# Kernel optimization log

Hardware: AMD Instinct MI355X
Metric: run time of the kernel (lower is better)

Reference implementation:

```python
import jax, jax.numpy as jnp
import numpy as np

N_NODES = 100000
N_EDGES = 1600000
D_IN = 128
D_OUT = 128


def setup_inputs() -> dict:
    key = jax.random.key(0)
    k1, k2, k3, k4, k5 = jax.random.split(key, 5)
    h = jax.random.normal(k1, (N_NODES, D_IN), dtype=jnp.float32)
    src = jax.random.randint(k2, (N_EDGES,), 0, N_NODES, dtype=jnp.int64)
    dst = jax.random.randint(k3, (N_EDGES,), 0, N_NODES, dtype=jnp.int64)
    # Glorot-ish init for linear weights (PyTorch nn.Linear style: [out, in])
    scale = 1.0 / np.sqrt(D_IN)
    W_self = jax.random.uniform(k4, (D_OUT, D_IN), jnp.float32, -scale, scale)
    W_neigh = jax.random.uniform(k5, (D_OUT, D_IN), jnp.float32, -scale, scale)
    b = jnp.zeros((D_OUT,), dtype=jnp.float32)
    return {"h": h, "src": src, "dst": dst, "W_self": W_self,
            "W_neigh": W_neigh, "b": b}


def reference(h, src, dst, W_self, W_neigh, b):
    n_nodes = h.shape[0]
    # neighbor gather + segment-mean over in-neighbors (DGL fn.copy_u + fn.mean)
    msg = h[src]                                            # [E, D_in]
    neigh_sum = jax.ops.segment_sum(msg, dst, num_segments=n_nodes)
    deg = jax.ops.segment_sum(jnp.ones_like(dst, dtype=h.dtype), dst,
                              num_segments=n_nodes)         # [N]
    h_neigh = neigh_sum / jnp.maximum(deg, 1.0)[:, None]    # mean; 0 for isolated
    # SAGEConv mean: fc_self(h) + fc_neigh(h_neigh) + bias
    out = h @ W_self.T + h_neigh @ W_neigh.T + b
    return out
```

## Files before the change

### kernel.cpp

```cpp
#include <hip/hip_runtime.h>
#include <stdint.h>

#define NN 100000
#define NE 1600000
#define DD 128
#define NTILES ((NN + 127) / 128)
#define NB 256
#define CHUNK (NE / NB)
#define NBUCK ((NN + 255) / 256)
#define GH_N (NBUCK * NB)
#define GH_BLK (GH_N / 256)

typedef __bf16 bf16x8 __attribute__((ext_vector_type(8)));
typedef float f32x4 __attribute__((ext_vector_type(4)));
typedef float f32x2 __attribute__((ext_vector_type(2)));

__device__ __forceinline__ unsigned int f2bf2(float a, float b) {
  union { float f; unsigned u; } x, y;
  x.f = a; y.f = b;
  unsigned ua = x.u + (0x7FFFu + ((x.u >> 16) & 1u));
  unsigned ub = y.u + (0x7FFFu + ((y.u >> 16) & 1u));
  return (ua >> 16) | (ub & 0xFFFF0000u);
}

__global__ __launch_bounds__(256) void convert_h8_kernel(const float4* __restrict__ hp,
                                                         uint2* __restrict__ h8) {
  int gid = blockIdx.x * 256 + threadIdx.x;
  float4 a = hp[2 * gid], b = hp[2 * gid + 1];
  int lo = __builtin_amdgcn_cvt_pk_fp8_f32(a.x, a.y, 0, false);
  lo = __builtin_amdgcn_cvt_pk_fp8_f32(a.z, a.w, lo, true);
  int hi = __builtin_amdgcn_cvt_pk_fp8_f32(b.x, b.y, 0, false);
  hi = __builtin_amdgcn_cvt_pk_fp8_f32(b.z, b.w, hi, true);
  h8[gid] = make_uint2((unsigned)lo, (unsigned)hi);
}

__global__ __launch_bounds__(256) void coarse_hist_kernel(const int* __restrict__ dst,
                                                          int* __restrict__ gh) {
  __shared__ int lh[NBUCK];
  int t = threadIdx.x, b = blockIdx.x;
  for (int i = t; i < NBUCK; i += 256) lh[i] = 0;
  __syncthreads();
  int e0 = b * CHUNK;
  for (int e = e0 + t; e < e0 + CHUNK; e += 256)
    atomicAdd(&lh[dst[e] >> 8], 1);
  __syncthreads();
  for (int i = t; i < NBUCK; i += 256) gh[i * NB + b] = lh[i];
}

__global__ __launch_bounds__(256) void blocksum_kernel(const int* __restrict__ gh,
                                                       int* __restrict__ bsum) {
  __shared__ int s[256];
  int t = threadIdx.x;
  s[t] = gh[blockIdx.x * 256 + t];
  __syncthreads();
  for (int d = 128; d > 0; d >>= 1) {
    if (t < d) s[t] += s[t + d];
    __syncthreads();
  }
  if (t == 0) bsum[blockIdx.x] = s[0];
}

__global__ __launch_bounds__(512) void scanbsum_kernel(const int* __restrict__ bsum,
                                                       int* __restrict__ bsum_ex) {
  __shared__ int s[512];
  int t = threadIdx.x;
  int v = (t < GH_BLK) ? bsum[t] : 0;
  s[t] = v;
  __syncthreads();
  for (int d = 1; d < 512; d <<= 1) {
    int x = (t >= d) ? s[t - d] : 0;
    __syncthreads();
    s[t] += x;
    __syncthreads();
  }
  if (t < GH_BLK) bsum_ex[t] = s[t] - v;
}

__global__ __launch_bounds__(256) void scanfull_kernel(const int* __restrict__ gh,
                                                       const int* __restrict__ bsum_ex,
                                                       int* __restrict__ gsc) {
  __shared__ int s[256];
  int t = threadIdx.x;
  int idx = blockIdx.x * 256 + t;
  int v = gh[idx];
  s[t] = v;
  __syncthreads();
  for (int d = 1; d < 256; d <<= 1) {
    int x = (t >= d) ? s[t - d] : 0;
    __syncthreads();
    s[t] += x;
    __syncthreads();
  }
  gsc[idx] = bsum_ex[blockIdx.x] + s[t] - v;
}

__global__ __launch_bounds__(256) void coarse_scatter_kernel(
    const int* __restrict__ src, const int* __restrict__ dst,
    const int* __restrict__ gsc, unsigned* __restrict__ ebuf) {
  __shared__ int lhpad[512];
  __shared__ int lbase[NBUCK];
  __shared__ int lcur[NBUCK];
  __shared__ int gstart[NBUCK];
  __shared__ unsigned sdata[CHUNK];
  __shared__ int sgpos[CHUNK];
  int t = threadIdx.x, b = blockIdx.x;
  lhpad[t] = 0;
  lhpad[t + 256] = 0;
  __syncthreads();
  int e0 = b * CHUNK;
  for (int e = e0 + t; e < e0 + CHUNK; e += 256)
    atomicAdd(&lhpad[dst[e] >> 8], 1);
  __syncthreads();
  int cnt0 = lhpad[t], cnt1 = lhpad[t + 256];
  for (int d = 1; d < 512; d <<= 1) {
    int x0 = (t >= d) ? lhpad[t - d] : 0;
    int x1 = ((t + 256) >= d) ? lhpad[t + 256 - d] : 0;
    __syncthreads();
    lhpad[t] += x0;
    lhpad[t + 256] += x1;
    __syncthreads();
  }
  if (t < NBUCK) { lbase[t] = lhpad[t] - cnt0; lcur[t] = 0; gstart[t] = gsc[t * NB + b]; }
  int i2 = t + 256;
  if (i2 < NBUCK) { lbase[i2] = lhpad[i2] - cnt1; lcur[i2] = 0; gstart[i2] = gsc[i2 * NB + b]; }
  __syncthreads();
  for (int e = e0 + t; e < e0 + CHUNK; e += 256) {
    int d = dst[e], s = src[e];
    int bk = d >> 8;
    int slot = atomicAdd(&lcur[bk], 1);
    int lp = lbase[bk] + slot;
    sdata[lp] = ((unsigned)(d & 255) << 24) | (unsigned)s;
    sgpos[lp] = gstart[bk] + slot;
  }
  __syncthreads();
  for (int j = t; j < CHUNK; j += 256) ebuf[sgpos[j]] = sdata[j];
}

__global__ __launch_bounds__(256) void fine_sort_kernel(const unsigned* __restrict__ ebuf,
                                                        const int* __restrict__ gsc,
                                                        int* __restrict__ csr,
                                                        int* __restrict__ offs) {
  __shared__ int hist[256], scn[256], cur[256];
  int t = threadIdx.x, g = blockIdx.x;
  int base = gsc[g * NB];
  int end = (g == NBUCK - 1) ? NE : gsc[(g + 1) * NB];
  hist[t] = 0;
  __syncthreads();
  for (int j = base + t; j < end; j += 256)
    atomicAdd(&hist[ebuf[j] >> 24], 1);
  __syncthreads();
  int v = hist[t];
  scn[t] = v;
  __syncthreads();
  for (int d = 1; d < 256; d <<= 1) {
    int x = (t >= d) ? scn[t - d] : 0;
    __syncthreads();
    scn[t] += x;
    __syncthreads();
  }
  int excl = scn[t] - v;
  int node = g * 256 + t;
  if (node < NN) offs[node] = base + excl;
  if (node == NN - 1) offs[NN] = NE;
  cur[t] = excl;
  __syncthreads();
  for (int j = base + t; j < end; j += 256) {
    unsigned p = ebuf[j];
    int pos = atomicAdd(&cur[p >> 24], 1);
    csr[base + pos] = (int)(p & 0x00FFFFFFu);
  }
}

__device__ __forceinline__ void acc16(float* a, uint4 u) {
  f32x2 p;
  p = __builtin_amdgcn_cvt_pk_f32_fp8(u.x, false); a[0] += p.x;  a[1] += p.y;
  p = __builtin_amdgcn_cvt_pk_f32_fp8(u.x, true);  a[2] += p.x;  a[3] += p.y;
  p = __builtin_amdgcn_cvt_pk_f32_fp8(u.y, false); a[4] += p.x;  a[5] += p.y;
  p = __builtin_amdgcn_cvt_pk_f32_fp8(u.y, true);  a[6] += p.x;  a[7] += p.y;
  p = __builtin_amdgcn_cvt_pk_f32_fp8(u.z, false); a[8] += p.x;  a[9] += p.y;
  p = __builtin_amdgcn_cvt_pk_f32_fp8(u.z, true);  a[10] += p.x; a[11] += p.y;
  p = __builtin_amdgcn_cvt_pk_f32_fp8(u.w, false); a[12] += p.x; a[13] += p.y;
  p = __builtin_amdgcn_cvt_pk_f32_fp8(u.w, true);  a[14] += p.x; a[15] += p.y;
}

__global__ __launch_bounds__(256) void gather_kernel(const uint4* __restrict__ h8,
                                                     const int* __restrict__ offs,
                                                     const int* __restrict__ csr,
                                                     uint4* __restrict__ hneighbf4) {
  int q = (blockIdx.x * 256 + threadIdx.x) >> 3;
  int l = threadIdx.x & 7;
  if (q >= NN) return;
  int off0 = offs[q], off1 = offs[q + 1];
  float a[16];
#pragma unroll
  for (int i = 0; i < 16; i++) a[i] = 0.f;
  int j = off0;
  for (; j + 4 <= off1; j += 4) {
    int s0 = csr[j], s1 = csr[j + 1], s2 = csr[j + 2], s3 = csr[j + 3];
    uint4 u0 = h8[(size_t)s0 * 8 + l];
    uint4 u1 = h8[(size_t)s1 * 8 + l];
    uint4 u2 = h8[(size_t)s2 * 8 + l];
    uint4 u3 = h8[(size_t)s3 * 8 + l];
    acc16(a, u0); acc16(a, u1); acc16(a, u2); acc16(a, u3);
  }
  for (; j < off1; j++) acc16(a, h8[(size_t)csr[j] * 8 + l]);
  int deg = off1 - off0;
  float sc = (deg > 0) ? (1.0f / (float)deg) : 0.0f;
  uint4 r0, r1;
  r0.x = f2bf2(a[0] * sc, a[1] * sc);   r0.y = f2bf2(a[2] * sc, a[3] * sc);
  r0.z = f2bf2(a[4] * sc, a[5] * sc);   r0.w = f2bf2(a[6] * sc, a[7] * sc);
  r1.x = f2bf2(a[8] * sc, a[9] * sc);   r1.y = f2bf2(a[10] * sc, a[11] * sc);
  r1.z = f2bf2(a[12] * sc, a[13] * sc); r1.w = f2bf2(a[14] * sc, a[15] * sc);
  hneighbf4[(size_t)q * 16 + 2 * l] = r0;
  hneighbf4[(size_t)q * 16 + 2 * l + 1] = r1;
}

__device__ __forceinline__ void stage_f32(const float* __restrict__ X,
                                          int row0, int nvalid,
                                          uint4* buf, int t) {
#pragma unroll
  for (int i = 0; i < 8; i++) {
    int id = t + (i << 8);
    int r = id >> 4;
    int c8 = id & 15;
    int row = row0 + r;
    float4 v0 = {0.f, 0.f, 0.f, 0.f}, v1 = {0.f, 0.f, 0.f, 0.f};
    if (row < nvalid) {
      const float4* p = (const float4*)(X + (size_t)row * DD + (c8 << 3));
      v0 = p[0];
      v1 = p[1];
    }
    uint4 q;
    q.x = f2bf2(v0.x, v0.y);
    q.y = f2bf2(v0.z, v0.w);
    q.z = f2bf2(v1.x, v1.y);
    q.w = f2bf2(v1.z, v1.w);
    int rt = r >> 4, m = r & 15, kc = c8 >> 2, quad = c8 & 3;
    buf[(((rt << 2) + kc) << 6) + (quad << 4) + m] = q;
  }
}

__device__ __forceinline__ void stage_bf(const uint4* __restrict__ X,
                                         int row0, int nvalid,
                                         uint4* buf, int t) {
#pragma unroll
  for (int i = 0; i < 8; i++) {
    int d = t + (i << 8);
    int rt = d >> 8, kc = (d >> 6) & 3, quad = (d >> 4) & 3, m = d & 15;
    int r = rt * 16 + m, c8 = kc * 4 + quad;
    int row = row0 + r;
    uint4 q = {0u, 0u, 0u, 0u};
    if (row < nvalid) q = X[(size_t)row * 16 + c8];
    buf[d] = q;
  }
}

__device__ __forceinline__ void compute_half(const uint4* sA, const uint4* sW,
                                             f32x4 acc[2][8], int wv, int lane) {
#pragma unroll
  for (int kc = 0; kc < 4; kc++) {
    bf16x8 b[8];
#pragma unroll
    for (int n = 0; n < 8; n++)
      b[n] = *(const bf16x8*)&sW[(((n << 2) + kc) << 6) + lane];
    bf16x8 a0 = *(const bf16x8*)&sA[((((wv * 2 + 0) << 2) + kc) << 6) + lane];
    bf16x8 a1 = *(const bf16x8*)&sA[((((wv * 2 + 1) << 2) + kc) << 6) + lane];
#pragma unroll
    for (int n = 0; n < 8; n++) {
      acc[0][n] = __builtin_amdgcn_mfma_f32_16x16x32_bf16(a0, b[n], acc[0][n], 0, 0, 0);
      acc[1][n] = __builtin_amdgcn_mfma_f32_16x16x32_bf16(a1, b[n], acc[1][n], 0, 0, 0);
    }
  }
}

__global__ __launch_bounds__(256) void gemm_kernel(
    const float* __restrict__ h, const uint4* __restrict__ hneighbf,
    const float* __restrict__ Wself, const float* __restrict__ Wneigh,
    const float* __restrict__ bias, float* __restrict__ out) {
  __shared__ uint4 sA[2048];
  __shared__ uint4 sW[2048];
  int t = threadIdx.x;
  int wv = t >> 6;
  int lane = t & 63;
  int row0 = blockIdx.x * 128;

  f32x4 acc[2][8];
#pragma unroll
  for (int i = 0; i < 2; i++)
#pragma unroll
    for (int n = 0; n < 8; n++) acc[i][n] = f32x4{0.f, 0.f, 0.f, 0.f};

  stage_f32(h, row0, NN, sA, t);
  stage_f32(Wself, 0, 128, sW, t);
  __syncthreads();
  compute_half(sA, sW, acc, wv, lane);
  __syncthreads();

  stage_bf(hneighbf, row0, NN, sA, t);
  stage_f32(Wneigh, 0, 128, sW, t);
  __syncthreads();
  compute_half(sA, sW, acc, wv, lane);

  int col = lane & 15, rq = lane >> 4;
  float bv[8];
#pragma unroll
  for (int n = 0; n < 8; n++) bv[n] = bias[n * 16 + col];
#pragma unroll
  for (int rt = 0; rt < 2; rt++) {
    int rb = row0 + (wv * 2 + rt) * 16 + rq * 4;
#pragma unroll
    for (int r = 0; r < 4; r++) {
      int row = rb + r;
      if (row < NN) {
        float* op = out + (size_t)row * DD + col;
#pragma unroll
        for (int n = 0; n < 8; n++) op[n * 16] = acc[rt][n][r] + bv[n];
      }
    }
  }
}

extern "C" void kernel_launch(void* const* d_in, const int* in_sizes, int n_in,
                              void* d_out, int out_size, void* d_ws, size_t ws_size,
                              hipStream_t stream) {
  const float* h      = (const float*)d_in[0];
  const int*   src    = (const int*)d_in[1];
  const int*   dst    = (const int*)d_in[2];
  const float* Wself  = (const float*)d_in[3];
  const float* Wneigh = (const float*)d_in[4];
  const float* bias   = (const float*)d_in[5];
  float* out = (float*)d_out;

  char* ws = (char*)d_ws;
  unsigned* h8       = (unsigned*)ws;
  unsigned* hneighbf = (unsigned*)(ws + 12800000);
  unsigned* ebuf     = (unsigned*)(ws + 12800000);
  int*      csr      = (int*)(ws + 38400000);
  int*      gh       = (int*)(ws + 44800000);
  int*      gsc      = (int*)(ws + 45200384);
  int*      bsum     = (int*)(ws + 45600768);
  int*      bsum_ex  = (int*)(ws + 45602336);
  int*      offs     = (int*)(ws + 45603904);

  convert_h8_kernel<<<6250, 256, 0, stream>>>((const float4*)h, (uint2*)h8);
  coarse_hist_kernel<<<NB, 256, 0, stream>>>(dst, gh);
  blocksum_kernel<<<GH_BLK, 256, 0, stream>>>(gh, bsum);
  scanbsum_kernel<<<1, 512, 0, stream>>>(bsum, bsum_ex);
  scanfull_kernel<<<GH_BLK, 256, 0, stream>>>(gh, bsum_ex, gsc);
  coarse_scatter_kernel<<<NB, 256, 0, stream>>>(src, dst, gsc, ebuf);
  fine_sort_kernel<<<NBUCK, 256, 0, stream>>>(ebuf, gsc, csr, offs);
  gather_kernel<<<(NN * 8 + 255) / 256, 256, 0, stream>>>(
      (const uint4*)h8, offs, csr, (uint4*)hneighbf);
  gemm_kernel<<<NTILES, 256, 0, stream>>>(h, (const uint4*)hneighbf,
                                          Wself, Wneigh, bias, out);
}
```

Before: 227.8 us.

## Fuse neighbor gather into GEMM and merge histogram into convert kernel

The neighbor mean-gather now runs inside the GEMM kernel and writes bf16 rows straight into shared memory, so the hneighbf intermediate is never written to or read back from global memory. The coarse histogram is folded into the fp8 conversion kernel, with its first 256 blocks doing the histogram work, to save one launch. In exchange the gather now runs in only 782 GEMM blocks, which may lower memory-level parallelism for the random gathers, and it adds a launch_bounds occupancy hint of 2.

```diff
diff --git a/kernel.cpp b/kernel.cpp
--- a/kernel.cpp
+++ b/kernel.cpp
@@ -23,8 +23,10 @@
   return (ua >> 16) | (ub & 0xFFFF0000u);
 }
 
-__global__ __launch_bounds__(256) void convert_h8_kernel(const float4* __restrict__ hp,
-                                                         uint2* __restrict__ h8) {
+__global__ __launch_bounds__(256) void convert_hist_kernel(
+    const float4* __restrict__ hp, uint2* __restrict__ h8,
+    const int* __restrict__ dst, int* __restrict__ gh) {
+  __shared__ int lh[NBUCK];
   int gid = blockIdx.x * 256 + threadIdx.x;
   float4 a = hp[2 * gid], b = hp[2 * gid + 1];
   int lo = __builtin_amdgcn_cvt_pk_fp8_f32(a.x, a.y, 0, false);
@@ -32,19 +34,17 @@
   int hi = __builtin_amdgcn_cvt_pk_fp8_f32(b.x, b.y, 0, false);
   hi = __builtin_amdgcn_cvt_pk_fp8_f32(b.z, b.w, hi, true);
   h8[gid] = make_uint2((unsigned)lo, (unsigned)hi);
-}
-
-__global__ __launch_bounds__(256) void coarse_hist_kernel(const int* __restrict__ dst,
-                                                          int* __restrict__ gh) {
-  __shared__ int lh[NBUCK];
-  int t = threadIdx.x, b = blockIdx.x;
-  for (int i = t; i < NBUCK; i += 256) lh[i] = 0;
-  __syncthreads();
-  int e0 = b * CHUNK;
-  for (int e = e0 + t; e < e0 + CHUNK; e += 256)
-    atomicAdd(&lh[dst[e] >> 8], 1);
-  __syncthreads();
-  for (int i = t; i < NBUCK; i += 256) gh[i * NB + b] = lh[i];
+
+  if (blockIdx.x < NB) {
+    int t = threadIdx.x, bb = blockIdx.x;
+    for (int i = t; i < NBUCK; i += 256) lh[i] = 0;
+    __syncthreads();
+    int e0 = bb * CHUNK;
+    for (int e = e0 + t; e < e0 + CHUNK; e += 256)
+      atomicAdd(&lh[dst[e] >> 8], 1);
+    __syncthreads();
+    for (int i = t; i < NBUCK; i += 256) gh[i * NB + bb] = lh[i];
+  }
 }
 
 __global__ __launch_bounds__(256) void blocksum_kernel(const int* __restrict__ gh,
@@ -181,38 +181,6 @@
   p = __builtin_amdgcn_cvt_pk_f32_fp8(u.z, true);  a[10] += p.x; a[11] += p.y;
   p = __builtin_amdgcn_cvt_pk_f32_fp8(u.w, false); a[12] += p.x; a[13] += p.y;
   p = __builtin_amdgcn_cvt_pk_f32_fp8(u.w, true);  a[14] += p.x; a[15] += p.y;
-}
-
-__global__ __launch_bounds__(256) void gather_kernel(const uint4* __restrict__ h8,
-                                                     const int* __restrict__ offs,
-                                                     const int* __restrict__ csr,
-                                                     uint4* __restrict__ hneighbf4) {
-  int q = (blockIdx.x * 256 + threadIdx.x) >> 3;
-  int l = threadIdx.x & 7;
-  if (q >= NN) return;
-  int off0 = offs[q], off1 = offs[q + 1];
-  float a[16];
-#pragma unroll
-  for (int i = 0; i < 16; i++) a[i] = 0.f;
-  int j = off0;
-  for (; j + 4 <= off1; j += 4) {
-    int s0 = csr[j], s1 = csr[j + 1], s2 = csr[j + 2], s3 = csr[j + 3];
-    uint4 u0 = h8[(size_t)s0 * 8 + l];
-    uint4 u1 = h8[(size_t)s1 * 8 + l];
-    uint4 u2 = h8[(size_t)s2 * 8 + l];
-    uint4 u3 = h8[(size_t)s3 * 8 + l];
-    acc16(a, u0); acc16(a, u1); acc16(a, u2); acc16(a, u3);
-  }
-  for (; j < off1; j++) acc16(a, h8[(size_t)csr[j] * 8 + l]);
-  int deg = off1 - off0;
-  float sc = (deg > 0) ? (1.0f / (float)deg) : 0.0f;
-  uint4 r0, r1;
-  r0.x = f2bf2(a[0] * sc, a[1] * sc);   r0.y = f2bf2(a[2] * sc, a[3] * sc);
-  r0.z = f2bf2(a[4] * sc, a[5] * sc);   r0.w = f2bf2(a[6] * sc, a[7] * sc);
-  r1.x = f2bf2(a[8] * sc, a[9] * sc);   r1.y = f2bf2(a[10] * sc, a[11] * sc);
-  r1.z = f2bf2(a[12] * sc, a[13] * sc); r1.w = f2bf2(a[14] * sc, a[15] * sc);
-  hneighbf4[(size_t)q * 16 + 2 * l] = r0;
-  hneighbf4[(size_t)q * 16 + 2 * l + 1] = r1;
 }
 
 __device__ __forceinline__ void stage_f32(const float* __restrict__ X,
@@ -240,21 +208,6 @@
   }
 }
 
-__device__ __forceinline__ void stage_bf(const uint4* __restrict__ X,
-                                         int row0, int nvalid,
-                                         uint4* buf, int t) {
-#pragma unroll
-  for (int i = 0; i < 8; i++) {
-    int d = t + (i << 8);
-    int rt = d >> 8, kc = (d >> 6) & 3, quad = (d >> 4) & 3, m = d & 15;
-    int r = rt * 16 + m, c8 = kc * 4 + quad;
-    int row = row0 + r;
-    uint4 q = {0u, 0u, 0u, 0u};
-    if (row < nvalid) q = X[(size_t)row * 16 + c8];
-    buf[d] = q;
-  }
-}
-
 __device__ __forceinline__ void compute_half(const uint4* sA, const uint4* sW,
                                              f32x4 acc[2][8], int wv, int lane) {
 #pragma unroll
@@ -273,8 +226,9 @@
   }
 }
 
-__global__ __launch_bounds__(256) void gemm_kernel(
-    const float* __restrict__ h, const uint4* __restrict__ hneighbf,
+__global__ __launch_bounds__(256, 2) void gemm_fused_kernel(
+    const float* __restrict__ h, const uint4* __restrict__ h8,
+    const int* __restrict__ offs, const int* __restrict__ csr,
     const float* __restrict__ Wself, const float* __restrict__ Wneigh,
     const float* __restrict__ bias, float* __restrict__ out) {
   __shared__ uint4 sA[2048];
@@ -296,8 +250,43 @@
   compute_half(sA, sW, acc, wv, lane);
   __syncthreads();
 
-  stage_bf(hneighbf, row0, NN, sA, t);
   stage_f32(Wneigh, 0, 128, sW, t);
+
+  int grp = t >> 3;
+  int l = t & 7;
+#pragma unroll 1
+  for (int rnd = 0; rnd < 4; rnd++) {
+    int r = rnd * 32 + grp;
+    int q = row0 + r;
+    float a[16];
+#pragma unroll
+    for (int i = 0; i < 16; i++) a[i] = 0.f;
+    float sc = 0.f;
+    if (q < NN) {
+      int off0 = offs[q], off1 = offs[q + 1];
+      int j = off0;
+      for (; j + 4 <= off1; j += 4) {
+        int s0 = csr[j], s1 = csr[j + 1], s2 = csr[j + 2], s3 = csr[j + 3];
+        uint4 u0 = h8[(size_t)s0 * 8 + l];
+        uint4 u1 = h8[(size_t)s1 * 8 + l];
+        uint4 u2 = h8[(size_t)s2 * 8 + l];
+        uint4 u3 = h8[(size_t)s3 * 8 + l];
+        acc16(a, u0); acc16(a, u1); acc16(a, u2); acc16(a, u3);
+      }
+      for (; j < off1; j++) acc16(a, h8[(size_t)csr[j] * 8 + l]);
+      int deg = off1 - off0;
+      sc = (deg > 0) ? (1.0f / (float)deg) : 0.0f;
+    }
+    uint4 r0, r1;
+    r0.x = f2bf2(a[0] * sc, a[1] * sc);   r0.y = f2bf2(a[2] * sc, a[3] * sc);
+    r0.z = f2bf2(a[4] * sc, a[5] * sc);   r0.w = f2bf2(a[6] * sc, a[7] * sc);
+    r1.x = f2bf2(a[8] * sc, a[9] * sc);   r1.y = f2bf2(a[10] * sc, a[11] * sc);
+    r1.z = f2bf2(a[12] * sc, a[13] * sc); r1.w = f2bf2(a[14] * sc, a[15] * sc);
+    int rt = r >> 4, m = r & 15;
+    int c8a = 2 * l, c8b = 2 * l + 1;
+    sA[(((rt << 2) + (c8a >> 2)) << 6) + ((c8a & 3) << 4) + m] = r0;
+    sA[(((rt << 2) + (c8b >> 2)) << 6) + ((c8b & 3) << 4) + m] = r1;
+  }
   __syncthreads();
   compute_half(sA, sW, acc, wv, lane);
 
@@ -333,7 +322,6 @@
 
   char* ws = (char*)d_ws;
   unsigned* h8       = (unsigned*)ws;
-  unsigned* hneighbf = (unsigned*)(ws + 12800000);
   unsigned* ebuf     = (unsigned*)(ws + 12800000);
   int*      csr      = (int*)(ws + 38400000);
   int*      gh       = (int*)(ws + 44800000);
@@ -342,15 +330,12 @@
   int*      bsum_ex  = (int*)(ws + 45602336);
   int*      offs     = (int*)(ws + 45603904);
 
-  convert_h8_kernel<<<6250, 256, 0, stream>>>((const float4*)h, (uint2*)h8);
-  coarse_hist_kernel<<<NB, 256, 0, stream>>>(dst, gh);
+  convert_hist_kernel<<<6250, 256, 0, stream>>>((const float4*)h, (uint2*)h8, dst, gh);
   blocksum_kernel<<<GH_BLK, 256, 0, stream>>>(gh, bsum);
   scanbsum_kernel<<<1, 512, 0, stream>>>(bsum, bsum_ex);
   scanfull_kernel<<<GH_BLK, 256, 0, stream>>>(gh, bsum_ex, gsc);
   coarse_scatter_kernel<<<NB, 256, 0, stream>>>(src, dst, gsc, ebuf);
   fine_sort_kernel<<<NBUCK, 256, 0, stream>>>(ebuf, gsc, csr, offs);
-  gather_kernel<<<(NN * 8 + 255) / 256, 256, 0, stream>>>(
-      (const uint4*)h8, offs, csr, (uint4*)hneighbf);
-  gemm_kernel<<<NTILES, 256, 0, stream>>>(h, (const uint4*)hneighbf,
-                                          Wself, Wneigh, bias, out);
-}
+  gemm_fused_kernel<<<NTILES, 256, 0, stream>>>(h, (const uint4*)h8, offs, csr,
+                                                Wself, Wneigh, bias, out);
+}
```

Result: slower. 234.2 us (+2.8%).
